# Optimization experiments

Hardware: AMD Instinct MI355X
Metric: run time of the kernel (lower is better)

## Reference

```python
import jax, jax.numpy as jnp
import numpy as np

G, NB, C, K, R, S = 5, 5, 64, 3, 8, 2   # n_groups, n_blocks, n_feats, kernel, reduction, scale
MOCO = 256


def setup_inputs() -> dict:
    key = jax.random.key(0)
    ks = iter(jax.random.split(key, 32))
    def rn(shape, s=0.02):
        return jax.random.normal(next(ks), shape, jnp.float32) * s
    return {
        "x": jax.random.normal(next(ks), (16, 3, 64, 64), jnp.float32),
        "k_v": jax.random.normal(next(ks), (16, MOCO), jnp.float32),
        "head_w": rn((C, 3, K, K)), "head_b": rn((C,)),
        "comp_w": rn((C, MOCO)),
        # DA_conv params, stacked over [group, block, which-of-2]
        "da_kw1": rn((G, NB, 2, C, C)),
        "da_kw2": rn((G, NB, 2, C * K * K, C)),
        "da_cw": rn((G, NB, 2, C, C)), "da_cb": rn((G, NB, 2, C)),
        "ca_w1": rn((G, NB, 2, C // R, C)), "ca_w2": rn((G, NB, 2, C, C // R)),
        # DAB plain 3x3 convs (conv1, conv2)
        "dab_cw": rn((G, NB, 2, C, C, K, K)), "dab_cb": rn((G, NB, 2, C)),
        # per-group tail conv, body tail conv, upsampler, final conv
        "grp_w": rn((G, C, C, K, K)), "grp_b": rn((G, C)),
        "body_w": rn((C, C, K, K)), "body_b": rn((C,)),
        "up_w": rn((C * S * S, C, K, K)), "up_b": rn((C * S * S,)),
        "tail_w": rn((3, C, K, K)), "tail_b": rn((3,)),
    }


def lrelu(x):
    return jax.nn.leaky_relu(x, 0.1)


def conv2d(x, w, b):
    p = (K - 1) // 2
    y = jax.lax.conv_general_dilated(x, w, (1, 1), [(p, p), (p, p)],
                                     dimension_numbers=("NCHW", "OIHW", "NCHW"))
    return y + b[None, :, None, None]


def da_conv(x, kv, kw1, kw2, cw, cb, caw1, caw2):
    # x: [B,C,H,W], kv: [B,C]
    B, Ch, H, W = x.shape
    # per-sample, per-channel dynamic KxK kernel (torch: groups=B*C depthwise conv)
    ker = (lrelu(kv @ kw1.T) @ kw2.T).reshape(B, Ch, K, K)
    p = (K - 1) // 2
    xp = jnp.pad(x, ((0, 0), (0, 0), (p, p), (p, p)))
    out = jnp.zeros_like(x)
    for i in range(K):
        for j in range(K):
            out = out + ker[:, :, i, j, None, None] * xp[:, :, i:i + H, j:j + W]
    out = lrelu(out)
    # 1x1 conv (with bias)
    out = jnp.einsum("bchw,oc->bohw", out, cw) + cb[None, :, None, None]
    # CA gate on kv (two bias-free 1x1 convs on 1x1 spatial == matmuls)
    att = jax.nn.sigmoid(lrelu(kv @ caw1.T) @ caw2.T)  # [B,C]
    return out + x * att[:, :, None, None]


def pixel_shuffle(t, r):
    B, Ct, H, W = t.shape
    c = Ct // (r * r)
    return t.reshape(B, c, r, r, H, W).transpose(0, 1, 4, 2, 5, 3).reshape(B, c, H * r, W * r)


def _forward(x, k_v, head_w, head_b, comp_w, da_kw1, da_kw2, da_cw, da_cb,
             ca_w1, ca_w2, dab_cw, dab_cb, grp_w, grp_b, body_w, body_b,
             up_w, up_b, tail_w, tail_b):
    kv = lrelu(k_v @ comp_w.T)            # compress: [B, C]
    x0 = conv2d(x, head_w, head_b)        # head
    res = x0
    for g in range(G):                    # DAGs
        gin = res
        for n in range(NB):               # DABs
            bin_ = res
            out = lrelu(da_conv(res, kv, da_kw1[g, n, 0], da_kw2[g, n, 0],
                                da_cw[g, n, 0], da_cb[g, n, 0], ca_w1[g, n, 0], ca_w2[g, n, 0]))
            out = lrelu(conv2d(out, dab_cw[g, n, 0], dab_cb[g, n, 0]))
            out = lrelu(da_conv(out, kv, da_kw1[g, n, 1], da_kw2[g, n, 1],
                                da_cw[g, n, 1], da_cb[g, n, 1], ca_w1[g, n, 1], ca_w2[g, n, 1]))
            res = conv2d(out, dab_cw[g, n, 1], dab_cb[g, n, 1]) + bin_
        res = conv2d(res, grp_w[g], grp_b[g]) + gin
    res = conv2d(res, body_w, body_b) + x0
    t = pixel_shuffle(conv2d(res, up_w, up_b), S)   # Upsampler (scale=2)
    return conv2d(t, tail_w, tail_b)


def reference(x, k_v, head_w, head_b, comp_w, da_kw1, da_kw2, da_cw, da_cb,
              ca_w1, ca_w2, dab_cw, dab_cb, grp_w, grp_b, body_w, body_b,
              up_w, up_b, tail_w, tail_b):
    return _forward(x, k_v, head_w, head_b, comp_w, da_kw1, da_kw2, da_cw, da_cb,
                    ca_w1, ca_w2, dab_cw, dab_cb, grp_w, grp_b, body_w, body_b,
                    up_w, up_b, tail_w, tail_b)
```

## Files before the change

### kernel.cpp

```cpp
#include <hip/hip_runtime.h>
#include <math.h>

#define DEV __device__ __forceinline__

DEV float lrelu_f(float v) { return v > 0.f ? v : 0.1f * v; }

DEV unsigned short f2bf(float f) {
    unsigned u = __builtin_bit_cast(unsigned, f);
    unsigned r = u + 0x7FFFu + ((u >> 16) & 1u);
    return (unsigned short)(r >> 16);
}

DEV float bf2f(unsigned short s) {
    return __builtin_bit_cast(float, (unsigned)s << 16);
}

typedef __attribute__((ext_vector_type(8))) short bh8;
typedef __attribute__((ext_vector_type(16))) float f16acc;

#define MFMA32(acc, a, b) acc = __builtin_amdgcn_mfma_f32_32x32x16_bf16(a, b, acc, 0, 0, 0)

__global__ void transpose_w(const float* __restrict__ src, float* __restrict__ dst,
                            int L, int O, int KK) {
    int idx = blockIdx.x * 256 + threadIdx.x;
    int tot = L * O * KK;
    if (idx >= tot) return;
    int l = idx / (O * KK);
    int r = idx - l * (O * KK);
    int o = r / KK;
    int k = r - o * KK;
    dst[((size_t)l * KK + k) * O + o] = src[idx];
}

__global__ void pack3x3(const float* __restrict__ src, unsigned short* __restrict__ dst, int L) {
    int idx = blockIdx.x * 256 + threadIdx.x;
    if (idx >= L * 4608) return;
    int l = idx / 4608;
    int r = idx - l * 4608;
    int c = r >> 7;
    int rr = r & 127;
    int nt = rr >> 6, lane = rr & 63;
    int o = nt * 32 + (lane & 31);
    int kg = lane >> 5;
    unsigned short v[8];
#pragma unroll
    for (int j = 0; j < 8; ++j) {
        int k = c * 16 + kg * 8 + j;
        int t = k >> 6, cin = k & 63;
        v[j] = f2bf(src[(((size_t)l * 64 + o) * 64 + cin) * 9 + t]);
    }
    uint4 u;
    u.x = v[0] | ((unsigned)v[1] << 16);
    u.y = v[2] | ((unsigned)v[3] << 16);
    u.z = v[4] | ((unsigned)v[5] << 16);
    u.w = v[6] | ((unsigned)v[7] << 16);
    *(uint4*)(dst + (size_t)idx * 8) = u;
}

__global__ void pack_da(const float* __restrict__ src, unsigned short* __restrict__ dst, int L) {
    int idx = blockIdx.x * 256 + threadIdx.x;
    if (idx >= L * 512) return;
    int l = idx >> 9;
    int r = idx & 511;
    int c = r >> 7;
    int rr = r & 127;
    int nt = rr >> 6, lane = rr & 63;
    int o = nt * 32 + (lane & 31);
    int kg = lane >> 5;
    unsigned short v[8];
#pragma unroll
    for (int j = 0; j < 8; ++j) {
        int cin = c * 16 + kg * 8 + j;
        v[j] = f2bf(src[((size_t)l * 64 + o) * 64 + cin]);
    }
    uint4 u;
    u.x = v[0] | ((unsigned)v[1] << 16);
    u.y = v[2] | ((unsigned)v[3] << 16);
    u.z = v[4] | ((unsigned)v[5] << 16);
    u.w = v[6] | ((unsigned)v[7] << 16);
    *(uint4*)(dst + (size_t)idx * 8) = u;
}

__global__ void pack_up(const float* __restrict__ src, unsigned short* __restrict__ dst) {
    int idx = blockIdx.x * 256 + threadIdx.x;
    if (idx >= 18432) return;
    int c = idx >> 9;
    int nt = (idx >> 6) & 7;
    int lane = idx & 63;
    int o = nt * 32 + (lane & 31);
    int kg = lane >> 5;
    unsigned short v[8];
#pragma unroll
    for (int j = 0; j < 8; ++j) {
        int k = c * 16 + kg * 8 + j;
        int t = k >> 6, cin = k & 63;
        v[j] = f2bf(src[((size_t)o * 64 + cin) * 9 + t]);
    }
    uint4 u;
    u.x = v[0] | ((unsigned)v[1] << 16);
    u.y = v[2] | ((unsigned)v[3] << 16);
    u.z = v[4] | ((unsigned)v[5] << 16);
    u.w = v[6] | ((unsigned)v[7] << 16);
    *(uint4*)(dst + (size_t)idx * 8) = u;
}

__global__ void pack_tail(const float* __restrict__ src, unsigned short* __restrict__ dst) {
    int idx = blockIdx.x * 256 + threadIdx.x;
    if (idx >= 2304) return;
    int c = idx >> 6;
    int lane = idx & 63;
    int o = lane & 31;
    int kg = lane >> 5;
    unsigned short v[8];
#pragma unroll
    for (int j = 0; j < 8; ++j) {
        int k = c * 16 + kg * 8 + j;
        int t = k >> 6, cin = k & 63;
        v[j] = (o < 3) ? f2bf(src[((size_t)o * 64 + cin) * 9 + t]) : (unsigned short)0;
    }
    uint4 u;
    u.x = v[0] | ((unsigned)v[1] << 16);
    u.y = v[2] | ((unsigned)v[3] << 16);
    u.z = v[4] | ((unsigned)v[5] << 16);
    u.w = v[6] | ((unsigned)v[7] << 16);
    *(uint4*)(dst + (size_t)idx * 8) = u;
}

__global__ void kv_kernel(const float* __restrict__ kvin, const float* __restrict__ comp_w,
                          float* __restrict__ kv) {
    int b = blockIdx.x, c = threadIdx.x;
    const float* a = kvin + b * 256;
    const float* w = comp_w + c * 256;
    float s = 0.f;
    for (int m = 0; m < 256; ++m) s += a[m] * w[m];
    kv[b * 64 + c] = lrelu_f(s);
}

__global__ void kerprep(const float* __restrict__ kv, const float* __restrict__ kw1,
                        const float* __restrict__ kw2, const float* __restrict__ caw1,
                        const float* __restrict__ caw2, float* __restrict__ ker_all,
                        float* __restrict__ att_all) {
    int l = blockIdx.x >> 4;
    int b = blockIdx.x & 15;
    int c = threadIdx.x;
    __shared__ float kvb[64];
    __shared__ float t1[64];
    __shared__ float a1[8];
    kvb[c] = kv[b * 64 + c];
    __syncthreads();
    {
        const float* w1 = kw1 + (size_t)l * 4096 + c * 64;
        float s = 0.f;
        for (int j = 0; j < 64; ++j) s += kvb[j] * w1[j];
        t1[c] = lrelu_f(s);
    }
    if (c < 8) {
        const float* cw1 = caw1 + (size_t)l * 512 + c * 64;
        float s = 0.f;
        for (int j = 0; j < 64; ++j) s += kvb[j] * cw1[j];
        a1[c] = lrelu_f(s);
    }
    __syncthreads();
    const float* w2 = kw2 + (size_t)l * 576 * 64;
    for (int t = 0; t < 9; ++t) {
        const float* row = w2 + (size_t)(c * 9 + t) * 64;
        float s = 0.f;
        for (int j = 0; j < 64; ++j) s += t1[j] * row[j];
        ker_all[(((size_t)l * 16 + b) * 9 + t) * 64 + c] = s;
    }
    {
        const float* c2 = caw2 + (size_t)l * 512 + c * 8;
        float s = 0.f;
        for (int r = 0; r < 8; ++r) s += a1[r] * c2[r];
        att_all[((size_t)l * 16 + b) * 64 + c] = 1.f / (1.f + expf(-s));
    }
}

__global__ __launch_bounds__(256) void head_conv(const float* __restrict__ x,
                                                 const float* __restrict__ wt,
                                                 const float* __restrict__ bias,
                                                 float* __restrict__ x0,
                                                 float* __restrict__ res,
                                                 unsigned short* __restrict__ resS) {
    int t = threadIdx.x;
    int co = t & 63, q = t >> 6;
    int bid = blockIdx.x;
    int b = bid >> 7;
    int rem = bid & 127;
    int y = rem >> 1;
    int xs = (rem & 1) * 32 + q * 8;

    float bv = bias[co];
    float acc[8];
#pragma unroll
    for (int p = 0; p < 8; ++p) acc[p] = bv;

    int coff[10];
    bool cok[10];
#pragma unroll
    for (int i = 0; i < 10; ++i) {
        int col = xs - 1 + i;
        cok[i] = (col >= 0) && (col < 64);
        coff[i] = cok[i] ? col : 0;
    }
    for (int cin = 0; cin < 3; ++cin) {
#pragma unroll
        for (int ky = 0; ky < 3; ++ky) {
            int row = y + ky - 1;
            bool rok = (row >= 0) && (row < 64);
            const float* rp = x + ((size_t)(b * 3 + cin) * 64 + (rok ? row : 0)) * 64;
            float v[10];
#pragma unroll
            for (int i = 0; i < 10; ++i) v[i] = (rok && cok[i]) ? rp[coff[i]] : 0.f;
            const float* wp = wt + ((cin * 3 + ky) * 3) * 64 + co;
            float w0 = wp[0], w1 = wp[64], w2 = wp[128];
#pragma unroll
            for (int p = 0; p < 8; ++p) acc[p] += w0 * v[p] + w1 * v[p + 1] + w2 * v[p + 2];
        }
    }
    size_t ob = (((size_t)b * 64 + y) * 64 + xs) * 64 + co;
#pragma unroll
    for (int p = 0; p < 8; ++p) {
        x0[ob + (size_t)p * 64] = acc[p];
        res[ob + (size_t)p * 64] = acc[p];
        resS[ob + (size_t)p * 64] = f2bf(acc[p]);
    }
}

__global__ __launch_bounds__(256, 2) void conv3x3_mfma(const unsigned short* __restrict__ in,
                                                       const unsigned short* __restrict__ wp,
                                                       const float* __restrict__ bias,
                                                       const float* __restrict__ residF,
                                                       float* __restrict__ outF,
                                                       unsigned short* __restrict__ outB,
                                                       int act) {
    __shared__ unsigned short sm[180 * 72];
    int tid = threadIdx.x;
    int bid = blockIdx.x;
    int b = bid >> 5;
    int rem = bid & 31;
    int ty = rem >> 2, tx = rem & 3;
    const unsigned short* inb = in + (size_t)b * 262144;

    int lane = tid & 63, w = tid >> 6;
    const unsigned short* bp = wp + (size_t)lane * 8;

    bh8 q0[6], q1[6];
#pragma unroll
    for (int i = 0; i < 6; ++i) {
        q0[i] = *(const bh8*)&bp[(size_t)i * 1024];
        q1[i] = *(const bh8*)&bp[(size_t)i * 1024 + 512];
    }

    for (int i = tid; i < 1440; i += 256) {
        int px = i >> 3, c8 = i & 7;
        int hy = px / 18, hx = px - hy * 18;
        int row = ty * 8 + hy - 1, col = tx * 16 + hx - 1;
        uint4 u = make_uint4(0u, 0u, 0u, 0u);
        if (row >= 0 && row < 64 && col >= 0 && col < 64)
            u = *(const uint4*)(inb + (((size_t)row * 64 + col) * 64 + c8 * 8));
        *(uint4*)&sm[px * 72 + c8 * 8] = u;
    }
    __syncthreads();

    int l31 = lane & 31, kg8 = (lane >> 5) * 8;
    int p0 = w * 32 + l31;
    int ly0 = p0 >> 4, lx0 = p0 & 15;

    f16acc a0 = {0,0,0,0,0,0,0,0,0,0,0,0,0,0,0,0};
    f16acc a1 = a0;

#pragma unroll
    for (int c = 0; c < 36; ++c) {
        int t = c >> 2, cc = c & 3;
        int tyt = t / 3, txt = t - tyt * 3;
        int base = ((ly0 + tyt) * 18 + lx0 + txt) * 72 + cc * 16 + kg8;
        bh8 A = *(const bh8*)&sm[base];
        bh8 B0 = q0[c % 6], B1 = q1[c % 6];
        if (c + 6 < 36) {
            q0[c % 6] = *(const bh8*)&bp[(size_t)(c + 6) * 1024];
            q1[c % 6] = *(const bh8*)&bp[(size_t)(c + 6) * 1024 + 512];
        }
        MFMA32(a0, A, B0);
        MFMA32(a1, A, B1);
    }

    float bias0 = bias[l31], bias1 = bias[32 + l31];
    int hi = lane >> 5;
    size_t outb = (size_t)b * 262144;
#pragma unroll
    for (int r = 0; r < 16; ++r) {
        int rowm = (r & 3) + 8 * (r >> 2) + 4 * hi;
        int m = w * 32 + rowm;
        int gy = ty * 8 + (m >> 4), gx = tx * 16 + (m & 15);
        size_t i0 = outb + (((size_t)gy * 64 + gx) * 64);
        float v0 = a0[r] + bias0, v1 = a1[r] + bias1;
        if (residF) {
            v0 += residF[i0 + l31];
            v1 += residF[i0 + 32 + l31];
        }
        if (act) { v0 = lrelu_f(v0); v1 = lrelu_f(v1); }
        if (outF) {
            outF[i0 + l31] = v0;
            outF[i0 + 32 + l31] = v1;
        }
        if (outB) {
            outB[i0 + l31] = f2bf(v0);
            outB[i0 + 32 + l31] = f2bf(v1);
        }
    }
}

__global__ __launch_bounds__(256, 2) void dab_mfma(const unsigned short* __restrict__ in,
                                                   const unsigned short* __restrict__ wda,
                                                   const float* __restrict__ cb,
                                                   const float* __restrict__ kerT,
                                                   const float* __restrict__ attv,
                                                   const unsigned short* __restrict__ wconv,
                                                   const float* __restrict__ cbias,
                                                   const float* __restrict__ residF,
                                                   float* __restrict__ outF,
                                                   unsigned short* __restrict__ outB,
                                                   int act) {
    __shared__ unsigned short sin_[240 * 72];
    __shared__ unsigned short mid[192 * 72];
    int tid = threadIdx.x;
    int bid = blockIdx.x;
    int b = bid >> 5;
    int rem = bid & 31;
    int ty = rem >> 2, tx = rem & 3;
    const unsigned short* inb = in + (size_t)b * 262144;

    int lane = tid & 63, w = tid >> 6;
    int l31 = lane & 31, kg8 = (lane >> 5) * 8, hi = lane >> 5;

    bh8 dB0[4], dB1[4];
#pragma unroll
    for (int cc = 0; cc < 4; ++cc) {
        dB0[cc] = *(const bh8*)&wda[((size_t)(cc * 2 + 0) * 64 + lane) * 8];
        dB1[cc] = *(const bh8*)&wda[((size_t)(cc * 2 + 1) * 64 + lane) * 8];
    }

    for (int i = tid; i < 1920; i += 256) {
        int px = i >> 3, c8 = i & 7;
        int hy = px / 20, hx = px - hy * 20;
        int row = ty * 8 + hy - 2, col = tx * 16 + hx - 2;
        uint4 u = make_uint4(0u, 0u, 0u, 0u);
        if (row >= 0 && row < 64 && col >= 0 && col < 64)
            u = *(const uint4*)(inb + (((size_t)row * 64 + col) * 64 + c8 * 8));
        *(uint4*)&sin_[px * 72 + c8 * 8] = u;
    }
    __syncthreads();

    {
        int c2 = tid & 31, q = tid >> 5;
        const float* kb = kerT + (size_t)b * 576 + 2 * c2;
        float ka[9], kbv[9];
#pragma unroll
        for (int t = 0; t < 9; ++t) {
            ka[t] = kb[t * 64];
            kbv[t] = kb[t * 64 + 1];
        }
#pragma unroll
        for (int rr = 0; rr < 2; ++rr) {
            int my = (rr == 0) ? q : 8 + q;
            if (rr == 1 && q >= 2) break;
            float m0[18], m1[18];
#pragma unroll
            for (int xx = 0; xx < 18; ++xx) { m0[xx] = 0.f; m1[xx] = 0.f; }
#pragma unroll
            for (int ky = 0; ky < 3; ++ky) {
                int sr = my + ky;
                float va[20], vb[20];
#pragma unroll
                for (int i = 0; i < 20; ++i) {
                    unsigned u = *(const unsigned*)&sin_[(sr * 20 + i) * 72 + 2 * c2];
                    va[i] = bf2f((unsigned short)(u & 0xffffu));
                    vb[i] = bf2f((unsigned short)(u >> 16));
                }
                float k0a = ka[ky * 3], k1a = ka[ky * 3 + 1], k2a = ka[ky * 3 + 2];
                float k0b = kbv[ky * 3], k1b = kbv[ky * 3 + 1], k2b = kbv[ky * 3 + 2];
#pragma unroll
                for (int xx = 0; xx < 18; ++xx) {
                    m0[xx] += k0a * va[xx] + k1a * va[xx + 1] + k2a * va[xx + 2];
                    m1[xx] += k0b * vb[xx] + k1b * vb[xx + 1] + k2b * vb[xx + 2];
                }
            }
#pragma unroll
            for (int xx = 0; xx < 18; ++xx) {
                unsigned u = (unsigned)f2bf(lrelu_f(m0[xx])) |
                             ((unsigned)f2bf(lrelu_f(m1[xx])) << 16);
                *(unsigned*)&mid[(my * 18 + xx) * 72 + 2 * c2] = u;
            }
        }
    }
    __syncthreads();

    {
        float cb0 = cb[l31], cb1 = cb[32 + l31];
        float at0 = attv[b * 64 + l31], at1 = attv[b * 64 + 32 + l31];
        for (int mt = w; mt < 6; mt += 4) {
            f16acc a0 = {0,0,0,0,0,0,0,0,0,0,0,0,0,0,0,0};
            f16acc a1 = a0;
#pragma unroll
            for (int cc = 0; cc < 4; ++cc) {
                bh8 A = *(const bh8*)&mid[(mt * 32 + l31) * 72 + cc * 16 + kg8];
                MFMA32(a0, A, dB0[cc]);
                MFMA32(a1, A, dB1[cc]);
            }
#pragma unroll
            for (int r = 0; r < 16; ++r) {
                int rowm = (r & 3) + 8 * (r >> 2) + 4 * hi;
                int px = mt * 32 + rowm;
                if (px < 180) {
                    int my = px / 18, mx = px - my * 18;
                    int gy = ty * 8 + my - 1, gx = tx * 16 + mx - 1;
                    bool ok = (gy >= 0) && (gy < 64) && (gx >= 0) && (gx < 64);
                    int spx = (my + 1) * 20 + (mx + 1);
                    float i0v = bf2f(sin_[spx * 72 + l31]);
                    float i1v = bf2f(sin_[spx * 72 + 32 + l31]);
                    float v0 = lrelu_f(a0[r] + cb0 + i0v * at0);
                    float v1 = lrelu_f(a1[r] + cb1 + i1v * at1);
                    mid[px * 72 + l31] = ok ? f2bf(v0) : (unsigned short)0;
                    mid[px * 72 + 32 + l31] = ok ? f2bf(v1) : (unsigned short)0;
                }
            }
        }
    }

    const unsigned short* bp = wconv + (size_t)lane * 8;
    bh8 q0[6], q1[6];
#pragma unroll
    for (int i = 0; i < 6; ++i) {
        q0[i] = *(const bh8*)&bp[(size_t)i * 1024];
        q1[i] = *(const bh8*)&bp[(size_t)i * 1024 + 512];
    }
    __syncthreads();

    int p0 = w * 32 + l31;
    int ly0 = p0 >> 4, lx0 = p0 & 15;

    f16acc c0 = {0,0,0,0,0,0,0,0,0,0,0,0,0,0,0,0};
    f16acc c1 = c0;

#pragma unroll
    for (int c = 0; c < 36; ++c) {
        int t = c >> 2, cc = c & 3;
        int tyt = t / 3, txt = t - tyt * 3;
        int base = ((ly0 + tyt) * 18 + lx0 + txt) * 72 + cc * 16 + kg8;
        bh8 A = *(const bh8*)&mid[base];
        bh8 B0 = q0[c % 6], B1 = q1[c % 6];
        if (c + 6 < 36) {
            q0[c % 6] = *(const bh8*)&bp[(size_t)(c + 6) * 1024];
            q1[c % 6] = *(const bh8*)&bp[(size_t)(c + 6) * 1024 + 512];
        }
        MFMA32(c0, A, B0);
        MFMA32(c1, A, B1);
    }

    float bias0 = cbias[l31], bias1 = cbias[32 + l31];
    size_t outb = (size_t)b * 262144;
#pragma unroll
    for (int r = 0; r < 16; ++r) {
        int rowm = (r & 3) + 8 * (r >> 2) + 4 * hi;
        int m = w * 32 + rowm;
        int gy = ty * 8 + (m >> 4), gx = tx * 16 + (m & 15);
        size_t i0 = outb + (((size_t)gy * 64 + gx) * 64);
        float v0 = c0[r] + bias0, v1 = c1[r] + bias1;
        if (residF) {
            v0 += residF[i0 + l31];
            v1 += residF[i0 + 32 + l31];
        }
        if (act) { v0 = lrelu_f(v0); v1 = lrelu_f(v1); }
        if (outF) {
            outF[i0 + l31] = v0;
            outF[i0 + 32 + l31] = v1;
        }
        if (outB) {
            outB[i0 + l31] = f2bf(v0);
            outB[i0 + 32 + l31] = f2bf(v1);
        }
    }
}

__global__ __launch_bounds__(256, 2) void up_mfma(const unsigned short* __restrict__ in,
                                                  const unsigned short* __restrict__ wp,
                                                  const float* __restrict__ bias,
                                                  unsigned short* __restrict__ shuf) {
    __shared__ unsigned short sm[100 * 72];
    int tid = threadIdx.x;
    int bid = blockIdx.x;
    int b = bid >> 6;
    int t6 = bid & 63;
    int ty = t6 >> 3, tx = t6 & 7;
    const unsigned short* inb = in + (size_t)b * 262144;

    int lane = tid & 63, w = tid >> 6;
    const unsigned short* bp = wp + (size_t)(w * 2) * 512 + (size_t)lane * 8;

    bh8 q0[4], q1[4];
#pragma unroll
    for (int i = 0; i < 4; ++i) {
        q0[i] = *(const bh8*)&bp[(size_t)i * 4096];
        q1[i] = *(const bh8*)&bp[(size_t)i * 4096 + 512];
    }

    for (int i = tid; i < 800; i += 256) {
        int px = i >> 3, c8 = i & 7;
        int hy = px / 10, hx = px - hy * 10;
        int row = ty * 8 + hy - 1, col = tx * 8 + hx - 1;
        uint4 u = make_uint4(0u, 0u, 0u, 0u);
        if (row >= 0 && row < 64 && col >= 0 && col < 64)
            u = *(const uint4*)(inb + (((size_t)row * 64 + col) * 64 + c8 * 8));
        *(uint4*)&sm[px * 72 + c8 * 8] = u;
    }
    __syncthreads();

    int l31 = lane & 31, kg8 = (lane >> 5) * 8;
    int ly0 = l31 >> 3, lx0 = l31 & 7;

    f16acc a00 = {0,0,0,0,0,0,0,0,0,0,0,0,0,0,0,0};
    f16acc a01 = a00, a10 = a00, a11 = a00;

#pragma unroll
    for (int c = 0; c < 36; ++c) {
        int t = c >> 2, cc = c & 3;
        int tyt = t / 3, txt = t - tyt * 3;
        int base0 = ((ly0 + tyt) * 10 + lx0 + txt) * 72 + cc * 16 + kg8;
        int base1 = base0 + 2880;
        bh8 A0 = *(const bh8*)&sm[base0];
        bh8 A1 = *(const bh8*)&sm[base1];
        bh8 B0 = q0[c % 4], B1 = q1[c % 4];
        if (c + 4 < 36) {
            q0[c % 4] = *(const bh8*)&bp[(size_t)(c + 4) * 4096];
            q1[c % 4] = *(const bh8*)&bp[(size_t)(c + 4) * 4096 + 512];
        }
        MFMA32(a00, A0, B0);
        MFMA32(a01, A0, B1);
        MFMA32(a10, A1, B0);
        MFMA32(a11, A1, B1);
    }

    int co0 = w * 64 + l31, co1 = co0 + 32;
    float bias0 = bias[co0], bias1 = bias[co1];
    int ch0 = co0 >> 2, r10 = (co0 >> 1) & 1, r20 = co0 & 1;
    int ch1 = co1 >> 2, r11 = (co1 >> 1) & 1, r21 = co1 & 1;
    int hi = lane >> 5;
#pragma unroll
    for (int r = 0; r < 16; ++r) {
        int rowm = (r & 3) + 8 * (r >> 2) + 4 * hi;
#pragma unroll
        for (int mt = 0; mt < 2; ++mt) {
            int m = mt * 32 + rowm;
            int y = ty * 8 + (m >> 3), x = tx * 8 + (m & 7);
            float va = (mt == 0) ? a00[r] : a10[r];
            float vb = (mt == 0) ? a01[r] : a11[r];
            shuf[(((size_t)b * 128 + 2 * y + r10) * 128 + 2 * x + r20) * 64 + ch0] = f2bf(va + bias0);
            shuf[(((size_t)b * 128 + 2 * y + r11) * 128 + 2 * x + r21) * 64 + ch1] = f2bf(vb + bias1);
        }
    }
}

__global__ __launch_bounds__(256) void tail_mfma(const unsigned short* __restrict__ shuf,
                                                 const unsigned short* __restrict__ wp,
                                                 const float* __restrict__ bias,
                                                 float* __restrict__ outp) {
    __shared__ unsigned short sm[324 * 72];
    int tid = threadIdx.x;
    int bid = blockIdx.x;
    int b = bid >> 6;
    int rem = bid & 63;
    int ty = rem >> 3, tx = rem & 7;
    const unsigned short* sb = shuf + (size_t)b * 128 * 128 * 64;

    for (int i = tid; i < 2592; i += 256) {
        int px = i >> 3, c8 = i & 7;
        int hy = px / 18, hx = px - hy * 18;
        int row = ty * 16 + hy - 1, col = tx * 16 + hx - 1;
        uint4 u = make_uint4(0u, 0u, 0u, 0u);
        if (row >= 0 && row < 128 && col >= 0 && col < 128)
            u = *(const uint4*)(sb + (((size_t)row * 128 + col) * 64 + c8 * 8));
        *(uint4*)&sm[px * 72 + c8 * 8] = u;
    }
    __syncthreads();

    int lane = tid & 63, w = tid >> 6;
    int l31 = lane & 31, kg8 = (lane >> 5) * 8;
    int mbase = w * 64;
    int p0 = mbase + l31;
    int ly0 = p0 >> 4, lx0 = p0 & 15;

    f16acc a0 = {0,0,0,0,0,0,0,0,0,0,0,0,0,0,0,0};
    f16acc a1 = a0;

#pragma unroll
    for (int t = 0; t < 9; ++t) {
        int tyt = t / 3, txt = t - tyt * 3;
        int base0 = ((ly0 + tyt) * 18 + lx0 + txt) * 72 + kg8;
        int base1 = base0 + 2592;
#pragma unroll
        for (int cc = 0; cc < 4; ++cc) {
            int c = t * 4 + cc;
            bh8 A0 = *(const bh8*)&sm[base0 + cc * 16];
            bh8 A1 = *(const bh8*)&sm[base1 + cc * 16];
            bh8 B = *(const bh8*)&wp[((size_t)c * 64 + lane) * 8];
            MFMA32(a0, A0, B);
            MFMA32(a1, A1, B);
        }
    }

    if (l31 < 3) {
        float bv = bias[l31];
        int hi = lane >> 5;
        size_t ob = ((size_t)b * 3 + l31) * 16384;
#pragma unroll
        for (int r = 0; r < 16; ++r) {
            int rowm = (r & 3) + 8 * (r >> 2) + 4 * hi;
            int m0 = mbase + rowm;
            int gy0 = ty * 16 + (m0 >> 4), gx0 = tx * 16 + (m0 & 15);
            outp[ob + (size_t)gy0 * 128 + gx0] = a0[r] + bv;
            int m1 = m0 + 32;
            int gy1 = ty * 16 + (m1 >> 4), gx1 = tx * 16 + (m1 & 15);
            outp[ob + (size_t)gy1 * 128 + gx1] = a1[r] + bv;
        }
    }
}

extern "C" void kernel_launch(void* const* d_in, const int* in_sizes, int n_in,
                              void* d_out, int out_size, void* d_ws, size_t ws_size,
                              hipStream_t stream) {
    const float* x      = (const float*)d_in[0];
    const float* k_v    = (const float*)d_in[1];
    const float* head_w = (const float*)d_in[2];
    const float* head_b = (const float*)d_in[3];
    const float* comp_w = (const float*)d_in[4];
    const float* da_kw1 = (const float*)d_in[5];
    const float* da_kw2 = (const float*)d_in[6];
    const float* da_cw  = (const float*)d_in[7];
    const float* da_cb  = (const float*)d_in[8];
    const float* ca_w1  = (const float*)d_in[9];
    const float* ca_w2  = (const float*)d_in[10];
    const float* dab_cw = (const float*)d_in[11];
    const float* dab_cb = (const float*)d_in[12];
    const float* grp_w  = (const float*)d_in[13];
    const float* grp_b  = (const float*)d_in[14];
    const float* body_w = (const float*)d_in[15];
    const float* body_b = (const float*)d_in[16];
    const float* up_w   = (const float*)d_in[17];
    const float* up_b   = (const float*)d_in[18];
    const float* tail_w = (const float*)d_in[19];
    const float* tail_b = (const float*)d_in[20];

    char* base = (char*)d_ws;
    auto alloc = [&](size_t bytes) -> char* {
        char* p = base;
        base += (bytes + 255) & ~(size_t)255;
        return p;
    };
    unsigned short* wp_dab  = (unsigned short*)alloc((size_t)50 * 36864 * 2);
    unsigned short* wp_grp  = (unsigned short*)alloc((size_t)5 * 36864 * 2);
    unsigned short* wp_body = (unsigned short*)alloc((size_t)36864 * 2);
    unsigned short* wp_up   = (unsigned short*)alloc((size_t)147456 * 2);
    unsigned short* wp_da   = (unsigned short*)alloc((size_t)50 * 4096 * 2);
    unsigned short* wp_tail = (unsigned short*)alloc((size_t)18432 * 2);
    float* wT_head = (float*)alloc(1728 * 4);
    float* kvbuf   = (float*)alloc(1024 * 4);
    float* ker_all = (float*)alloc((size_t)460800 * 4);
    float* att_all = (float*)alloc((size_t)51200 * 4);
    const size_t ACT = (size_t)16 * 64 * 64 * 64;
    float* x0 = (float*)alloc(ACT * 4);
    float* rA = (float*)alloc(ACT * 4);
    float* rB = (float*)alloc(ACT * 4);
    float* rC = (float*)alloc(ACT * 4);
    unsigned short* sA = (unsigned short*)alloc(ACT * 2);
    unsigned short* sB = (unsigned short*)alloc(ACT * 2);
    unsigned short* sC = (unsigned short*)alloc(ACT * 2);
    unsigned short* t1 = (unsigned short*)alloc(ACT * 2);
    unsigned short* shuf = (unsigned short*)alloc((size_t)16 * 128 * 128 * 64 * 2);

    pack3x3<<<900, 256, 0, stream>>>(dab_cw, wp_dab, 50);
    pack3x3<<<90, 256, 0, stream>>>(grp_w, wp_grp, 5);
    pack3x3<<<18, 256, 0, stream>>>(body_w, wp_body, 1);
    pack_da<<<100, 256, 0, stream>>>(da_cw, wp_da, 50);
    pack_up<<<72, 256, 0, stream>>>(up_w, wp_up);
    pack_tail<<<9, 256, 0, stream>>>(tail_w, wp_tail);
    transpose_w<<<7, 256, 0, stream>>>(head_w, wT_head, 1, 64, 27);

    kv_kernel<<<16, 64, 0, stream>>>(k_v, comp_w, kvbuf);
    kerprep<<<800, 64, 0, stream>>>(kvbuf, da_kw1, da_kw2, ca_w1, ca_w2, ker_all, att_all);

    head_conv<<<2048, 256, 0, stream>>>(x, wT_head, head_b, x0, rA, sA);

    for (int g = 0; g < 5; ++g) {
        float* curF = rA;
        unsigned short* curS = sA;
        for (int n = 0; n < 5; ++n) {
            int l0 = (g * 5 + n) * 2, l1 = l0 + 1;
            dab_mfma<<<512, 256, 0, stream>>>(curS,
                                              wp_da + (size_t)l0 * 4096,
                                              da_cb + (size_t)l0 * 64,
                                              ker_all + (size_t)l0 * 9216,
                                              att_all + (size_t)l0 * 1024,
                                              wp_dab + (size_t)l0 * 36864,
                                              dab_cb + (size_t)l0 * 64,
                                              nullptr, nullptr, t1, 1);
            float* outF = (curF == rB) ? rC : rB;
            unsigned short* outS = (curS == sB) ? sC : sB;
            dab_mfma<<<512, 256, 0, stream>>>(t1,
                                              wp_da + (size_t)l1 * 4096,
                                              da_cb + (size_t)l1 * 64,
                                              ker_all + (size_t)l1 * 9216,
                                              att_all + (size_t)l1 * 1024,
                                              wp_dab + (size_t)l1 * 36864,
                                              dab_cb + (size_t)l1 * 64,
                                              curF, outF, outS, 0);
            curF = outF;
            curS = outS;
        }
        conv3x3_mfma<<<512, 256, 0, stream>>>(curS, wp_grp + (size_t)g * 36864,
                                              grp_b + (size_t)g * 64, rA, rC, sC, 0);
        float* tf = rA; rA = rC; rC = tf;
        unsigned short* ts = sA; sA = sC; sC = ts;
    }
    conv3x3_mfma<<<512, 256, 0, stream>>>(sA, wp_body, body_b, x0, nullptr, t1, 0);

    up_mfma<<<1024, 256, 0, stream>>>(t1, wp_up, up_b, shuf);
    tail_mfma<<<1024, 256, 0, stream>>>(shuf, wp_tail, tail_b, (float*)d_out);
}
```

Measured before the change: 1.524 ms.

## Swizzle LDS tiles with XOR layout and split warps across N/M tiles

Replaces the padded 72-element LDS row stride with a 64-element stride plus XOR swizzle of 8-element chunks in all conv kernels, which shrinks shared memory and aims to avoid bank conflicts. In conv3x3_mfma and dab_mfma the wave work split changes from each wave doing 32 pixels times 64 channels to each wave doing 64 pixels times 32 channels. Each wave then holds one B fragment stream instead of two, cutting weight-register pressure and global weight loads. The DAB conv weight prefetch is also hoisted to the start of the kernel, overlapping it with the earlier stages.

```diff
diff --git a/kernel.cpp b/kernel.cpp
--- a/kernel.cpp
+++ b/kernel.cpp
@@ -14,6 +14,8 @@
 DEV float bf2f(unsigned short s) {
     return __builtin_bit_cast(float, (unsigned)s << 16);
 }
+
+DEV int soff(int px, int c8) { return (px << 6) + (((c8 ^ (px & 7))) << 3); }
 
 typedef __attribute__((ext_vector_type(8))) short bh8;
 typedef __attribute__((ext_vector_type(16))) float f16acc;
@@ -234,7 +236,7 @@
                                                        float* __restrict__ outF,
                                                        unsigned short* __restrict__ outB,
                                                        int act) {
-    __shared__ unsigned short sm[180 * 72];
+    __shared__ unsigned short sm[180 * 64];
     int tid = threadIdx.x;
     int bid = blockIdx.x;
     int b = bid >> 5;
@@ -243,14 +245,12 @@
     const unsigned short* inb = in + (size_t)b * 262144;
 
     int lane = tid & 63, w = tid >> 6;
-    const unsigned short* bp = wp + (size_t)lane * 8;
-
-    bh8 q0[6], q1[6];
-#pragma unroll
-    for (int i = 0; i < 6; ++i) {
-        q0[i] = *(const bh8*)&bp[(size_t)i * 1024];
-        q1[i] = *(const bh8*)&bp[(size_t)i * 1024 + 512];
-    }
+    int nt = w >> 1, mp = w & 1;
+    const unsigned short* bp = wp + (size_t)nt * 512 + (size_t)lane * 8;
+
+    bh8 q[6];
+#pragma unroll
+    for (int i = 0; i < 6; ++i) q[i] = *(const bh8*)&bp[(size_t)i * 1024];
 
     for (int i = tid; i < 1440; i += 256) {
         int px = i >> 3, c8 = i & 7;
@@ -259,12 +259,12 @@
         uint4 u = make_uint4(0u, 0u, 0u, 0u);
         if (row >= 0 && row < 64 && col >= 0 && col < 64)
             u = *(const uint4*)(inb + (((size_t)row * 64 + col) * 64 + c8 * 8));
-        *(uint4*)&sm[px * 72 + c8 * 8] = u;
+        *(uint4*)&sm[soff(px, c8)] = u;
     }
     __syncthreads();
 
-    int l31 = lane & 31, kg8 = (lane >> 5) * 8;
-    int p0 = w * 32 + l31;
+    int l31 = lane & 31, hi = lane >> 5;
+    int p0 = mp * 64 + l31;
     int ly0 = p0 >> 4, lx0 = p0 & 15;
 
     f16acc a0 = {0,0,0,0,0,0,0,0,0,0,0,0,0,0,0,0};
@@ -274,40 +274,32 @@
     for (int c = 0; c < 36; ++c) {
         int t = c >> 2, cc = c & 3;
         int tyt = t / 3, txt = t - tyt * 3;
-        int base = ((ly0 + tyt) * 18 + lx0 + txt) * 72 + cc * 16 + kg8;
-        bh8 A = *(const bh8*)&sm[base];
-        bh8 B0 = q0[c % 6], B1 = q1[c % 6];
-        if (c + 6 < 36) {
-            q0[c % 6] = *(const bh8*)&bp[(size_t)(c + 6) * 1024];
-            q1[c % 6] = *(const bh8*)&bp[(size_t)(c + 6) * 1024 + 512];
-        }
-        MFMA32(a0, A, B0);
-        MFMA32(a1, A, B1);
-    }
-
-    float bias0 = bias[l31], bias1 = bias[32 + l31];
-    int hi = lane >> 5;
+        int hp0 = (ly0 + tyt) * 18 + lx0 + txt;
+        bh8 A0 = *(const bh8*)&sm[soff(hp0, cc * 2 + hi)];
+        bh8 A1 = *(const bh8*)&sm[soff(hp0 + 36, cc * 2 + hi)];
+        bh8 B = q[c % 6];
+        if (c + 6 < 36) q[c % 6] = *(const bh8*)&bp[(size_t)(c + 6) * 1024];
+        MFMA32(a0, A0, B);
+        MFMA32(a1, A1, B);
+    }
+
+    float bv = bias[nt * 32 + l31];
     size_t outb = (size_t)b * 262144;
+    int ch = nt * 32 + l31;
 #pragma unroll
     for (int r = 0; r < 16; ++r) {
         int rowm = (r & 3) + 8 * (r >> 2) + 4 * hi;
-        int m = w * 32 + rowm;
-        int gy = ty * 8 + (m >> 4), gx = tx * 16 + (m & 15);
-        size_t i0 = outb + (((size_t)gy * 64 + gx) * 64);
-        float v0 = a0[r] + bias0, v1 = a1[r] + bias1;
-        if (residF) {
-            v0 += residF[i0 + l31];
-            v1 += residF[i0 + 32 + l31];
-        }
+        int m0 = mp * 64 + rowm;
+        int m1 = m0 + 32;
+        int gy0 = ty * 8 + (m0 >> 4), gx0 = tx * 16 + (m0 & 15);
+        int gy1 = ty * 8 + (m1 >> 4), gx1 = tx * 16 + (m1 & 15);
+        size_t i0 = outb + (((size_t)gy0 * 64 + gx0) * 64) + ch;
+        size_t i1 = outb + (((size_t)gy1 * 64 + gx1) * 64) + ch;
+        float v0 = a0[r] + bv, v1 = a1[r] + bv;
+        if (residF) { v0 += residF[i0]; v1 += residF[i1]; }
         if (act) { v0 = lrelu_f(v0); v1 = lrelu_f(v1); }
-        if (outF) {
-            outF[i0 + l31] = v0;
-            outF[i0 + 32 + l31] = v1;
-        }
-        if (outB) {
-            outB[i0 + l31] = f2bf(v0);
-            outB[i0 + 32 + l31] = f2bf(v1);
-        }
+        if (outF) { outF[i0] = v0; outF[i1] = v1; }
+        if (outB) { outB[i0] = f2bf(v0); outB[i1] = f2bf(v1); }
     }
 }
 
@@ -322,8 +314,8 @@
                                                    float* __restrict__ outF,
                                                    unsigned short* __restrict__ outB,
                                                    int act) {
-    __shared__ unsigned short sin_[240 * 72];
-    __shared__ unsigned short mid[192 * 72];
+    __shared__ unsigned short sin_[240 * 64];
+    __shared__ unsigned short mid[192 * 64];
     int tid = threadIdx.x;
     int bid = blockIdx.x;
     int b = bid >> 5;
@@ -332,7 +324,8 @@
     const unsigned short* inb = in + (size_t)b * 262144;
 
     int lane = tid & 63, w = tid >> 6;
-    int l31 = lane & 31, kg8 = (lane >> 5) * 8, hi = lane >> 5;
+    int l31 = lane & 31, hi = lane >> 5;
+    int nt = w >> 1, mp = w & 1;
 
     bh8 dB0[4], dB1[4];
 #pragma unroll
@@ -340,6 +333,10 @@
         dB0[cc] = *(const bh8*)&wda[((size_t)(cc * 2 + 0) * 64 + lane) * 8];
         dB1[cc] = *(const bh8*)&wda[((size_t)(cc * 2 + 1) * 64 + lane) * 8];
     }
+    const unsigned short* bp = wconv + (size_t)nt * 512 + (size_t)lane * 8;
+    bh8 q[6];
+#pragma unroll
+    for (int i = 0; i < 6; ++i) q[i] = *(const bh8*)&bp[(size_t)i * 1024];
 
     for (int i = tid; i < 1920; i += 256) {
         int px = i >> 3, c8 = i & 7;
@@ -348,12 +345,12 @@
         uint4 u = make_uint4(0u, 0u, 0u, 0u);
         if (row >= 0 && row < 64 && col >= 0 && col < 64)
             u = *(const uint4*)(inb + (((size_t)row * 64 + col) * 64 + c8 * 8));
-        *(uint4*)&sin_[px * 72 + c8 * 8] = u;
+        *(uint4*)&sin_[soff(px, c8)] = u;
     }
     __syncthreads();
 
     {
-        int c2 = tid & 31, q = tid >> 5;
+        int c2 = tid & 31, qi = tid >> 5;
         const float* kb = kerT + (size_t)b * 576 + 2 * c2;
         float ka[9], kbv[9];
 #pragma unroll
@@ -361,10 +358,12 @@
             ka[t] = kb[t * 64];
             kbv[t] = kb[t * 64 + 1];
         }
+        int cchunk = c2 >> 2;
+        int cofs = 2 * (c2 & 3);
 #pragma unroll
         for (int rr = 0; rr < 2; ++rr) {
-            int my = (rr == 0) ? q : 8 + q;
-            if (rr == 1 && q >= 2) break;
+            int my = (rr == 0) ? qi : 8 + qi;
+            if (rr == 1 && qi >= 2) break;
             float m0[18], m1[18];
 #pragma unroll
             for (int xx = 0; xx < 18; ++xx) { m0[xx] = 0.f; m1[xx] = 0.f; }
@@ -374,7 +373,8 @@
                 float va[20], vb[20];
 #pragma unroll
                 for (int i = 0; i < 20; ++i) {
-                    unsigned u = *(const unsigned*)&sin_[(sr * 20 + i) * 72 + 2 * c2];
+                    int px = sr * 20 + i;
+                    unsigned u = *(const unsigned*)&sin_[soff(px, cchunk) + cofs];
                     va[i] = bf2f((unsigned short)(u & 0xffffu));
                     vb[i] = bf2f((unsigned short)(u >> 16));
                 }
@@ -388,9 +388,10 @@
             }
 #pragma unroll
             for (int xx = 0; xx < 18; ++xx) {
+                int px = my * 18 + xx;
                 unsigned u = (unsigned)f2bf(lrelu_f(m0[xx])) |
                              ((unsigned)f2bf(lrelu_f(m1[xx])) << 16);
-                *(unsigned*)&mid[(my * 18 + xx) * 72 + 2 * c2] = u;
+                *(unsigned*)&mid[soff(px, cchunk) + cofs] = u;
             }
         }
     }
@@ -399,12 +400,13 @@
     {
         float cb0 = cb[l31], cb1 = cb[32 + l31];
         float at0 = attv[b * 64 + l31], at1 = attv[b * 64 + 32 + l31];
+        int wch0 = l31 >> 3, wof = l31 & 7;
         for (int mt = w; mt < 6; mt += 4) {
             f16acc a0 = {0,0,0,0,0,0,0,0,0,0,0,0,0,0,0,0};
             f16acc a1 = a0;
 #pragma unroll
             for (int cc = 0; cc < 4; ++cc) {
-                bh8 A = *(const bh8*)&mid[(mt * 32 + l31) * 72 + cc * 16 + kg8];
+                bh8 A = *(const bh8*)&mid[soff(mt * 32 + l31, cc * 2 + hi)];
                 MFMA32(a0, A, dB0[cc]);
                 MFMA32(a1, A, dB1[cc]);
             }
@@ -417,27 +419,19 @@
                     int gy = ty * 8 + my - 1, gx = tx * 16 + mx - 1;
                     bool ok = (gy >= 0) && (gy < 64) && (gx >= 0) && (gx < 64);
                     int spx = (my + 1) * 20 + (mx + 1);
-                    float i0v = bf2f(sin_[spx * 72 + l31]);
-                    float i1v = bf2f(sin_[spx * 72 + 32 + l31]);
+                    float i0v = bf2f(sin_[soff(spx, wch0) + wof]);
+                    float i1v = bf2f(sin_[soff(spx, 4 + wch0) + wof]);
                     float v0 = lrelu_f(a0[r] + cb0 + i0v * at0);
                     float v1 = lrelu_f(a1[r] + cb1 + i1v * at1);
-                    mid[px * 72 + l31] = ok ? f2bf(v0) : (unsigned short)0;
-                    mid[px * 72 + 32 + l31] = ok ? f2bf(v1) : (unsigned short)0;
+                    mid[soff(px, wch0) + wof] = ok ? f2bf(v0) : (unsigned short)0;
+                    mid[soff(px, 4 + wch0) + wof] = ok ? f2bf(v1) : (unsigned short)0;
                 }
             }
         }
     }
-
-    const unsigned short* bp = wconv + (size_t)lane * 8;
-    bh8 q0[6], q1[6];
-#pragma unroll
-    for (int i = 0; i < 6; ++i) {
-        q0[i] = *(const bh8*)&bp[(size_t)i * 1024];
-        q1[i] = *(const bh8*)&bp[(size_t)i * 1024 + 512];
-    }
     __syncthreads();
 
-    int p0 = w * 32 + l31;
+    int p0 = mp * 64 + l31;
     int ly0 = p0 >> 4, lx0 = p0 & 15;
 
     f16acc c0 = {0,0,0,0,0,0,0,0,0,0,0,0,0,0,0,0};
@@ -447,39 +441,32 @@
     for (int c = 0; c < 36; ++c) {
         int t = c >> 2, cc = c & 3;
         int tyt = t / 3, txt = t - tyt * 3;
-        int base = ((ly0 + tyt) * 18 + lx0 + txt) * 72 + cc * 16 + kg8;
-        bh8 A = *(const bh8*)&mid[base];
-        bh8 B0 = q0[c % 6], B1 = q1[c % 6];
-        if (c + 6 < 36) {
-            q0[c % 6] = *(const bh8*)&bp[(size_t)(c + 6) * 1024];
-            q1[c % 6] = *(const bh8*)&bp[(size_t)(c + 6) * 1024 + 512];
-        }
-        MFMA32(c0, A, B0);
-        MFMA32(c1, A, B1);
-    }
-
-    float bias0 = cbias[l31], bias1 = cbias[32 + l31];
+        int hp0 = (ly0 + tyt) * 18 + lx0 + txt;
+        bh8 A0 = *(const bh8*)&mid[soff(hp0, cc * 2 + hi)];
+        bh8 A1 = *(const bh8*)&mid[soff(hp0 + 36, cc * 2 + hi)];
+        bh8 B = q[c % 6];
+        if (c + 6 < 36) q[c % 6] = *(const bh8*)&bp[(size_t)(c + 6) * 1024];
+        MFMA32(c0, A0, B);
+        MFMA32(c1, A1, B);
+    }
+
+    float bv = cbias[nt * 32 + l31];
     size_t outb = (size_t)b * 262144;
+    int ch = nt * 32 + l31;
 #pragma unroll
     for (int r = 0; r < 16; ++r) {
         int rowm = (r & 3) + 8 * (r >> 2) + 4 * hi;
-        int m = w * 32 + rowm;
-        int gy = ty * 8 + (m >> 4), gx = tx * 16 + (m & 15);
-        size_t i0 = outb + (((size_t)gy * 64 + gx) * 64);
-        float v0 = c0[r] + bias0, v1 = c1[r] + bias1;
-        if (residF) {
-            v0 += residF[i0 + l31];
-            v1 += residF[i0 + 32 + l31];
-        }
+        int m0 = mp * 64 + rowm;
+        int m1 = m0 + 32;
+        int gy0 = ty * 8 + (m0 >> 4), gx0 = tx * 16 + (m0 & 15);
+        int gy1 = ty * 8 + (m1 >> 4), gx1 = tx * 16 + (m1 & 15);
+        size_t i0 = outb + (((size_t)gy0 * 64 + gx0) * 64) + ch;
+        size_t i1 = outb + (((size_t)gy1 * 64 + gx1) * 64) + ch;
+        float v0 = c0[r] + bv, v1 = c1[r] + bv;
+        if (residF) { v0 += residF[i0]; v1 += residF[i1]; }
         if (act) { v0 = lrelu_f(v0); v1 = lrelu_f(v1); }
-        if (outF) {
-            outF[i0 + l31] = v0;
-            outF[i0 + 32 + l31] = v1;
-        }
-        if (outB) {
-            outB[i0 + l31] = f2bf(v0);
-            outB[i0 + 32 + l31] = f2bf(v1);
-        }
+        if (outF) { outF[i0] = v0; outF[i1] = v1; }
+        if (outB) { outB[i0] = f2bf(v0); outB[i1] = f2bf(v1); }
     }
 }
 
@@ -487,7 +474,7 @@
                                                   const unsigned short* __restrict__ wp,
                                                   const float* __restrict__ bias,
                                                   unsigned short* __restrict__ shuf) {
-    __shared__ unsigned short sm[100 * 72];
+    __shared__ unsigned short sm[100 * 64];
     int tid = threadIdx.x;
     int bid = blockIdx.x;
     int b = bid >> 6;
@@ -512,11 +499,11 @@
         uint4 u = make_uint4(0u, 0u, 0u, 0u);
         if (row >= 0 && row < 64 && col >= 0 && col < 64)
             u = *(const uint4*)(inb + (((size_t)row * 64 + col) * 64 + c8 * 8));
-        *(uint4*)&sm[px * 72 + c8 * 8] = u;
+        *(uint4*)&sm[soff(px, c8)] = u;
     }
     __syncthreads();
 
-    int l31 = lane & 31, kg8 = (lane >> 5) * 8;
+    int l31 = lane & 31, hi = lane >> 5;
     int ly0 = l31 >> 3, lx0 = l31 & 7;
 
     f16acc a00 = {0,0,0,0,0,0,0,0,0,0,0,0,0,0,0,0};
@@ -526,10 +513,9 @@
     for (int c = 0; c < 36; ++c) {
         int t = c >> 2, cc = c & 3;
         int tyt = t / 3, txt = t - tyt * 3;
-        int base0 = ((ly0 + tyt) * 10 + lx0 + txt) * 72 + cc * 16 + kg8;
-        int base1 = base0 + 2880;
-        bh8 A0 = *(const bh8*)&sm[base0];
-        bh8 A1 = *(const bh8*)&sm[base1];
+        int hp0 = (ly0 + tyt) * 10 + lx0 + txt;
+        bh8 A0 = *(const bh8*)&sm[soff(hp0, cc * 2 + hi)];
+        bh8 A1 = *(const bh8*)&sm[soff(hp0 + 40, cc * 2 + hi)];
         bh8 B0 = q0[c % 4], B1 = q1[c % 4];
         if (c + 4 < 36) {
             q0[c % 4] = *(const bh8*)&bp[(size_t)(c + 4) * 4096];
@@ -545,7 +531,6 @@
     float bias0 = bias[co0], bias1 = bias[co1];
     int ch0 = co0 >> 2, r10 = (co0 >> 1) & 1, r20 = co0 & 1;
     int ch1 = co1 >> 2, r11 = (co1 >> 1) & 1, r21 = co1 & 1;
-    int hi = lane >> 5;
 #pragma unroll
     for (int r = 0; r < 16; ++r) {
         int rowm = (r & 3) + 8 * (r >> 2) + 4 * hi;
@@ -565,7 +550,7 @@
                                                  const unsigned short* __restrict__ wp,
                                                  const float* __restrict__ bias,
                                                  float* __restrict__ outp) {
-    __shared__ unsigned short sm[324 * 72];
+    __shared__ unsigned short sm[324 * 64];
     int tid = threadIdx.x;
     int bid = blockIdx.x;
     int b = bid >> 6;
@@ -580,12 +565,12 @@
         uint4 u = make_uint4(0u, 0u, 0u, 0u);
         if (row >= 0 && row < 128 && col >= 0 && col < 128)
             u = *(const uint4*)(sb + (((size_t)row * 128 + col) * 64 + c8 * 8));
-        *(uint4*)&sm[px * 72 + c8 * 8] = u;
+        *(uint4*)&sm[soff(px, c8)] = u;
     }
     __syncthreads();
 
     int lane = tid & 63, w = tid >> 6;
-    int l31 = lane & 31, kg8 = (lane >> 5) * 8;
+    int l31 = lane & 31, hi = lane >> 5;
     int mbase = w * 64;
     int p0 = mbase + l31;
     int ly0 = p0 >> 4, lx0 = p0 & 15;
@@ -596,13 +581,12 @@
 #pragma unroll
     for (int t = 0; t < 9; ++t) {
         int tyt = t / 3, txt = t - tyt * 3;
-        int base0 = ((ly0 + tyt) * 18 + lx0 + txt) * 72 + kg8;
-        int base1 = base0 + 2592;
+        int hp0 = (ly0 + tyt) * 18 + lx0 + txt;
 #pragma unroll
         for (int cc = 0; cc < 4; ++cc) {
             int c = t * 4 + cc;
-            bh8 A0 = *(const bh8*)&sm[base0 + cc * 16];
-            bh8 A1 = *(const bh8*)&sm[base1 + cc * 16];
+            bh8 A0 = *(const bh8*)&sm[soff(hp0, cc * 2 + hi)];
+            bh8 A1 = *(const bh8*)&sm[soff(hp0 + 36, cc * 2 + hi)];
             bh8 B = *(const bh8*)&wp[((size_t)c * 64 + lane) * 8];
             MFMA32(a0, A0, B);
             MFMA32(a1, A1, B);
@@ -611,7 +595,6 @@
 
     if (l31 < 3) {
         float bv = bias[l31];
-        int hi = lane >> 5;
         size_t ob = ((size_t)b * 3 + l31) * 16384;
 #pragma unroll
         for (int r = 0; r < 16; ++r) {
```

Measured after the change: 1.888 ms. +23.8%, slower.
